# Kernel tuning notes

Measured on AMD Instinct MI355X. Metric: run time of the kernel, lower is better.

Reference implementation:

```python
import jax, jax.numpy as jnp
import numpy as np
from jax import lax

# Geometry constants (mirror ParallelGeometry with angle_ratio=1.0)
PHI_SIZE = 720
T_SIZE = 1024
N = 256            # reco_shape
B = 16             # batch
RHO = float(np.sqrt(2.0))          # ||max_pt - min_pt||/2 for [-1,1]^2
DT = 2.0 * RHO / T_SIZE            # detector step
A = -RHO                           # left edge used in phase factor
DPHI = np.pi / PHI_SIZE            # mean angle step (angle_ratio=1)


def setup_inputs() -> dict:
    key = jax.random.key(0)
    k1, k2, k3 = jax.random.split(key, 3)
    sinos = jax.random.normal(k1, (B, PHI_SIZE, T_SIZE), dtype=jnp.float32)
    kernel_re = jax.random.normal(k2, (T_SIZE // 2 + 1,), dtype=jnp.float32)
    kernel_im = jax.random.normal(k3, (T_SIZE // 2 + 1,), dtype=jnp.float32)
    return {"sinos": sinos, "kernel_re": kernel_re, "kernel_im": kernel_im}


def _filter_sinos(sinos, kernel):
    # fourier_transform (no padding): dt * exp(-i a w) * rfft(sinos)
    omgs = 2.0 * np.pi * jnp.fft.rfftfreq(T_SIZE, d=DT).astype(jnp.float32)  # [T/2+1]
    phase = jnp.exp(-1j * (A * omgs))          # cos(a w) - i sin(a w)
    sino_hat = (DT * phase) * jnp.fft.rfft(sinos, axis=-1)
    filtered_hat = kernel * sino_hat
    # inverse_fourier_transform: exp(+i a w)/dt * filtered_hat, then irfft
    back = (jnp.conj(phase) / DT) * filtered_hat
    return jnp.fft.irfft(back, n=T_SIZE, axis=-1)   # [B, phi, T], real


def _backproject(filtered):
    # Parallel-beam backprojection (ODL RayTransform adjoint):
    # f(x,y) = dphi * sum_phi lin_interp(g[phi], t = x cos(phi) + y sin(phi))
    angles = ((jnp.arange(PHI_SIZE, dtype=jnp.float32) + 0.5) * (np.pi / PHI_SIZE))
    xs = (-1.0 + (jnp.arange(N, dtype=jnp.float32) + 0.5) * (2.0 / N))  # pixel centers
    X, Y = jnp.meshgrid(xs, xs, indexing='ij')      # ODL axis order: [x, y]
    g_seq = jnp.transpose(filtered, (1, 0, 2))      # [phi, B, T]

    def step(acc, inp):
        g, phi = inp                                # g: [B, T]
        t = X * jnp.cos(phi) + Y * jnp.sin(phi)     # [N, N], always in [-rho, rho]
        u = (t + RHO) / DT - 0.5                    # fractional detector index
        i0 = jnp.clip(jnp.floor(u).astype(jnp.int32), 0, T_SIZE - 2)
        w = u - i0.astype(jnp.float32)
        val = g[:, i0] * (1.0 - w) + g[:, i0 + 1] * w   # [B, N, N]
        return acc + val, None

    acc0 = jnp.zeros((filtered.shape[0], N, N), dtype=filtered.dtype)
    acc, _ = lax.scan(step, acc0, (g_seq, angles))
    return acc * jnp.asarray(DPHI, dtype=filtered.dtype)


def reference(sinos, kernel_re, kernel_im):
    kernel = kernel_re.astype(jnp.complex64) + 1j * kernel_im.astype(jnp.complex64)
    filtered = _filter_sinos(sinos, kernel)
    return _backproject(filtered)
```

## Files before the change

### kernel.cpp

```cpp
#include <hip/hip_runtime.h>

#define PHI 720
#define TS 1024
#define NB 16
#define NPIX 256

#define INVDT 362.03867196751236f
#define DXF 0.0078125f
#define DPHI_F 0.0043633231299858237f

#define WS_TW 0
#define WS_ANG 4096
#define WS_PT 8192
#define WS_NEEDED (8192 + 256 * 360 * 16)

__device__ __forceinline__ float2 cmulf2(float2 a, float2 b) {
    return make_float2(a.x * b.x - a.y * b.y, a.x * b.y + a.y * b.x);
}
__device__ __forceinline__ float fract_fast(float x) {
#if __has_builtin(__builtin_amdgcn_fractf)
    return __builtin_amdgcn_fractf(x);
#else
    return x - floorf(x);
#endif
}

__global__ __launch_bounds__(256) void precompute_kernel(char* __restrict__ wsb) {
    const int blk = blockIdx.x, tid = threadIdx.x;
    if (blk < 360) {
        const int e = blk * 256 + tid;
        const unsigned repu = (unsigned)e / 360u;
        const int rep = (int)repu;
        const int a = e - rep * 360;
        const int ti = rep >> 4, tj = rep & 15;
        float s, c;
        sincosf(((float)a + 0.5f) * (3.14159265358979323846f / 720.0f), &s, &c);
        const float x0 = -1.0f + ((float)(ti * 8) + 0.5f) * DXF;
        const float x7 = x0 + 7.0f * DXF;
        const float y0 = -1.0f + ((float)(tj * 8) + 0.5f) * DXF;
        const float y7 = y0 + 7.0f * DXF;
        const float uTmin = (c * x0 + s * y0) * INVDT + 511.5f;
        const float uTmax = (c * x7 + s * y7) * INVDT + 511.5f;
        const float uUmin = (s * x0 - c * y7) * INVDT + 511.5f;
        const float uUmax = (s * x7 - c * y0) * INVDT + 511.5f;
        int wbA = (int)floorf(uTmin - 0.02f) - 1;
        int wbB = (int)floorf(1023.0f - uTmax - 0.02f) - 1;
        int wbC = (int)floorf(uUmin - 0.02f) - 1;
        int wbD = (int)floorf(1023.0f - uUmax - 0.02f) - 1;
        wbA = min(max(wbA, 0), 992);
        wbB = min(max(wbB, 0), 992);
        wbC = min(max(wbC, 0), 992);
        wbD = min(max(wbD, 0), 992);
        uint4 ent;
        ent.x = __float_as_uint(511.5f - (float)wbA);
        ent.y = __float_as_uint(511.5f - (float)wbC);
        ent.z = (unsigned)wbA | ((unsigned)wbB << 16);
        ent.w = (unsigned)wbC | ((unsigned)wbD << 16);
        ((uint4*)(wsb + WS_PT))[e] = ent;
    } else if (blk < 362) {
        const int k = (blk - 360) * 256 + tid;
        float s, c;
        sincosf((float)k * (6.28318530717958647692f / 1024.0f), &s, &c);
        ((float2*)(wsb + WS_TW))[k] = make_float2(c, -s);
    } else {
        const int a = (blk - 362) * 256 + tid;
        if (a < 360) {
            float s, c;
            sincosf(((float)a + 0.5f) * (3.14159265358979323846f / 720.0f), &s, &c);
            ((float2*)(wsb + WS_ANG))[a] = make_float2(c * INVDT, s * INVDT);
        }
    }
}

__device__ __forceinline__ void r4_stage(const float2* __restrict__ s0, float2* __restrict__ d0,
                                         const float2* __restrict__ s1, float2* __restrict__ d1,
                                         const float2* __restrict__ tw, int tid, int m, bool inv) {
    const int q = tid & ~(m - 1);
    const int o = tid + 3 * q;
    float2 w1 = tw[q], w2 = tw[2 * q];
    if (inv) { w1.y = -w1.y; w2.y = -w2.y; }
    #pragma unroll
    for (int f = 0; f < 2; ++f) {
        const float2* s = f ? s1 : s0;
        float2* d = f ? d1 : d0;
        const float2 a = s[tid], b = s[tid + 256], c = s[tid + 512], e = s[tid + 768];
        const float2 A = make_float2(a.x + c.x, a.y + c.y);
        const float2 Bm = cmulf2(w1, make_float2(a.x - c.x, a.y - c.y));
        const float2 C = make_float2(b.x + e.x, b.y + e.y);
        const float2 Dm = cmulf2(w1, make_float2(b.x - e.x, b.y - e.y));
        const float2 D = inv ? make_float2(-Dm.y, Dm.x) : make_float2(Dm.y, -Dm.x);
        d[o]         = make_float2(A.x + C.x, A.y + C.y);
        d[o + m]     = make_float2(Bm.x + D.x, Bm.y + D.y);
        d[o + 2 * m] = cmulf2(w2, make_float2(A.x - C.x, A.y - C.y));
        d[o + 3 * m] = cmulf2(w2, make_float2(Bm.x - D.x, Bm.y - D.y));
    }
}

__global__ __launch_bounds__(256) void filter_fft_kernel(float* __restrict__ sinos,
                                                         const float* __restrict__ kr,
                                                         const float* __restrict__ ki,
                                                         const char* __restrict__ wsb) {
    __shared__ float2 bufA[2][1024];
    __shared__ float2 bufB[2][1024];
    __shared__ float2 tw[512];
    const int tid = threadIdx.x;
    const int wg = blockIdx.x;
    const int lb = (wg & 7) * 360 + (wg >> 3);
    float* base = sinos + (size_t)lb * 4096;

    #pragma unroll
    for (int f = 0; f < 2; ++f) {
        float* r0 = base + f * 2048;
        float* r1 = r0 + 1024;
        #pragma unroll
        for (int h = 0; h < 4; ++h) {
            const int k = tid + h * 256;
            bufA[f][k] = make_float2(r0[k], r1[k]);
        }
    }
    if (wsb) {
        const float2* tg = (const float2*)(wsb + WS_TW);
        tw[tid] = tg[tid];
        tw[tid + 256] = tg[tid + 256];
    } else {
        #pragma unroll
        for (int h = 0; h < 2; ++h) {
            const int k = tid + h * 256;
            float s, c;
            sincosf((float)k * (6.28318530717958647692f / 1024.0f), &s, &c);
            tw[k] = make_float2(c, -s);
        }
    }
    __syncthreads();

    r4_stage(bufA[0], bufB[0], bufA[1], bufB[1], tw, tid, 1, false);   __syncthreads();
    r4_stage(bufB[0], bufA[0], bufB[1], bufA[1], tw, tid, 4, false);   __syncthreads();
    r4_stage(bufA[0], bufB[0], bufA[1], bufB[1], tw, tid, 16, false);  __syncthreads();
    r4_stage(bufB[0], bufA[0], bufB[1], bufA[1], tw, tid, 64, false);  __syncthreads();
    r4_stage(bufA[0], bufB[0], bufA[1], bufB[1], tw, tid, 256, false); __syncthreads();

    const float scale = DPHI_F / 1024.0f;
    #pragma unroll
    for (int h = 0; h < 4; ++h) {
        const int k = tid + h * 256;
        const int kk = (k <= 512) ? k : (1024 - k);
        const float re = kr[kk] * scale;
        float im = ((k == 0) || (k == 512)) ? 0.0f : ki[kk] * scale;
        if (k > 512) im = -im;
        #pragma unroll
        for (int f = 0; f < 2; ++f) {
            const float2 z = bufB[f][k];
            bufB[f][k] = make_float2(re * z.x - im * z.y, re * z.y + im * z.x);
        }
    }
    __syncthreads();

    r4_stage(bufB[0], bufA[0], bufB[1], bufA[1], tw, tid, 1, true);   __syncthreads();
    r4_stage(bufA[0], bufB[0], bufA[1], bufB[1], tw, tid, 4, true);   __syncthreads();
    r4_stage(bufB[0], bufA[0], bufB[1], bufA[1], tw, tid, 16, true);  __syncthreads();
    r4_stage(bufA[0], bufB[0], bufA[1], bufB[1], tw, tid, 64, true);  __syncthreads();
    r4_stage(bufB[0], bufA[0], bufB[1], bufA[1], tw, tid, 256, true); __syncthreads();

    #pragma unroll
    for (int f = 0; f < 2; ++f) {
        float* r0 = base + f * 2048;
        float* r1 = r0 + 1024;
        #pragma unroll
        for (int h = 0; h < 4; ++h) {
            const int k = tid + h * 256;
            const float2 v = bufA[f][k];
            r0[k] = v.x;
            r1[k] = v.y;
        }
    }
}

__global__ __launch_bounds__(64, 4) void backproj_sym_kernel(const float* __restrict__ filt,
                                                             float* __restrict__ out,
                                                             const char* __restrict__ wsb) {
    __shared__ float lds[2 * 4 * 256];
    const int l = threadIdx.x;
    const int wg = blockIdx.x;
    const int lb = ((wg & 7) << 9) | (wg >> 3);
    const int b = lb >> 8;
    const int rep = lb & 255;
    const int ti = rep >> 4, tj = rep & 15;

    const float2* __restrict__ ang = (const float2*)(wsb + WS_ANG);
    const uint4* __restrict__ pt = ((const uint4*)(wsb + WS_PT)) + rep * 360;

    const int ii = l >> 3, jj = l & 7;
    const int ip = ti * 8 + ii, jp = tj * 8 + jj;
    const float Xc = -1.0f + ((float)ip + 0.5f) * DXF;
    const float Yc = -1.0f + ((float)jp + 0.5f) * DXF;
    const int vbyte = ((l & 31) + ((l >> 5) * (360 * 1024))) * 4;
    const float* __restrict__ gb = filt + (size_t)b * (PHI * TS);

    float a0 = 0.f, a1 = 0.f, a2 = 0.f, a3 = 0.f;
    float pf[4][4];

#define STAGE(CH) { \
    _Pragma("unroll") \
    for (int p = 0; p < 4; ++p) { \
        const int ap = (CH) * 4 + p; \
        const uint4 e = pt[ap]; \
        const char* rp = (const char*)(gb + (ap << 10)); \
        pf[p][0] = *(const float*)(rp + ((e.z & 0xFFFFu) << 2) + vbyte); \
        pf[p][1] = *(const float*)(rp + ((e.z >> 16) << 2) + vbyte); \
        pf[p][2] = *(const float*)(rp + ((e.w & 0xFFFFu) << 2) + vbyte); \
        pf[p][3] = *(const float*)(rp + ((e.w >> 16) << 2) + vbyte); \
    } }

#define WRITE(BUF) { \
    _Pragma("unroll") \
    for (int p = 0; p < 4; ++p) { \
        _Pragma("unroll") \
        for (int w = 0; w < 4; ++w) \
            lds[(BUF) * 1024 + p * 256 + w * 64 + l] = pf[p][w]; \
    } }

#define COMPUTE(BUF, CH) { \
    _Pragma("unroll") \
    for (int p = 0; p < 4; ++p) { \
        const int ap = (CH) * 4 + p; \
        const uint4 e = pt[ap]; \
        const float2 cs = ang[ap]; \
        const float* slot = &lds[(BUF) * 1024 + p * 256]; \
        const float kFA = __uint_as_float(e.x), kFC = __uint_as_float(e.y); \
        const int wbA = (int)(e.z & 0xFFFFu), wbB = (int)(e.z >> 16); \
        const int wbC = (int)(e.w & 0xFFFFu), wbD = (int)(e.w >> 16); \
        const float uT = fmaf(cs.x, Xc, fmaf(cs.y, Yc, kFA)); \
        const float uU = fmaf(cs.y, Xc, fmaf(cs.x, -Yc, kFC)); \
        const int iA = (int)uT; const float wT = fract_fast(uT); \
        const int iC = (int)uU; const float wU = fract_fast(uU); \
        const int iB = 1022 - wbA - wbB - iA; \
        const int iD = 1022 - wbC - wbD - iC; \
        { const float g0 = slot[iA],       g1 = slot[iA + 1]; \
          const float h0 = slot[iA + 32],  h1 = slot[iA + 33]; \
          a0 = fmaf(wT, g1 - g0, a0 + g0); a1 = fmaf(wT, h1 - h0, a1 + h0); } \
        { const float g0 = slot[64 + iB],  g1 = slot[65 + iB]; \
          const float h0 = slot[96 + iB],  h1 = slot[97 + iB]; \
          a2 = fmaf(wT, g0 - g1, a2 + g1); a3 = fmaf(wT, h0 - h1, a3 + h1); } \
        { const float g0 = slot[128 + iC], g1 = slot[129 + iC]; \
          const float h0 = slot[160 + iC], h1 = slot[161 + iC]; \
          a1 = fmaf(wU, g1 - g0, a1 + g0); a2 = fmaf(wU, h1 - h0, a2 + h0); } \
        { const float g0 = slot[192 + iD], g1 = slot[193 + iD]; \
          const float h0 = slot[224 + iD], h1 = slot[225 + iD]; \
          a3 = fmaf(wU, g0 - g1, a3 + g1); a0 = fmaf(wU, h0 - h1, a0 + h1); } \
    } }

    STAGE(0); WRITE(0);
    for (int cc = 0; cc < 44; ++cc) {
        STAGE(2 * cc + 1);
        COMPUTE(0, 2 * cc);
        WRITE(1);
        STAGE(2 * cc + 2);
        COMPUTE(1, 2 * cc + 1);
        WRITE(0);
    }
    STAGE(89);
    COMPUTE(0, 88);
    WRITE(1);
    COMPUTE(1, 89);

#undef STAGE
#undef WRITE
#undef COMPUTE

    const int bb = b << 8;
    out[((size_t)((bb + ip) << 8)) + jp]                    = a0;
    out[((size_t)((bb + 255 - jp) << 8)) + ip]              = a1;
    out[((size_t)((bb + 255 - ip) << 8)) + (255 - jp)]      = a2;
    out[((size_t)((bb + jp) << 8)) + (255 - ip)]            = a3;
}

__global__ __launch_bounds__(256) void backproj_fb_kernel(const float* __restrict__ filt,
                                                          float* __restrict__ out) {
    __shared__ float2 csI[PHI];
    __shared__ float win[8 * 128];
    __shared__ float woffF[8];

    const int tid = threadIdx.x;
    const int wg = blockIdx.x;
    const int lb = ((wg & 7) << 7) | (wg >> 3);
    const int b = lb >> 6;
    const int tile = lb & 63;
    const int i0 = (tile >> 3) * 32;
    const int j0 = (tile & 7) * 32;

    for (int p = tid; p < PHI; p += 256) {
        const float angv = ((float)p + 0.5f) * (float)(3.14159265358979323846 / 720.0);
        float s, c;
        sincosf(angv, &s, &c);
        csI[p] = make_float2(c * INVDT, s * INVDT);
    }

    const int lane = tid & 63;
    const int wv = tid >> 6;
    const int ii = lane & 7;
    const int jj = lane >> 3;
    const int ipx = i0 + ii;
    const int j = j0 + wv * 8 + jj;

    const float Xc = -1.0f + ((float)ipx + 0.5f) * DXF;
    const float Yc = -1.0f + ((float)j + 0.5f) * DXF;

    const int r = tid >> 5;
    const int l32 = tid & 31;
    const float xlo = -1.0f + ((float)i0 + 0.5f) * DXF;
    const float xhi = -1.0f + ((float)i0 + 31.5f) * DXF;
    const float ylo = -1.0f + ((float)j0 + 0.5f) * DXF;
    const float yhi = -1.0f + ((float)j0 + 31.5f) * DXF;

    const float* gb = filt + (size_t)b * PHI * TS;
    float acc0 = 0.f, acc1 = 0.f, acc2 = 0.f, acc3 = 0.f;

    __syncthreads();

    {
        const float2 cs = csI[r];
        const float um = fminf(cs.x * xlo, cs.x * xhi) + fminf(cs.y * ylo, cs.y * yhi) + 511.5f;
        const int wb = (int)floorf(um) - 1;
        const float* grow = gb + (size_t)r * TS;
        #pragma unroll
        for (int h = 0; h < 4; ++h) {
            int gi = wb + l32 + 32 * h;
            gi = gi < 0 ? 0 : (gi > TS - 1 ? TS - 1 : gi);
            win[r * 128 + l32 + 32 * h] = grow[gi];
        }
        if (l32 == 0) woffF[r] = 511.5f + (float)(r * 128 - wb);
    }
    __syncthreads();

    for (int c = 0; c < PHI / 8; ++c) {
        float gp0 = 0.f, gp1 = 0.f, gp2 = 0.f, gp3 = 0.f;
        int wbn = 0;
        const bool more = (c + 1 < PHI / 8);
        if (more) {
            const int a = (c + 1) * 8 + r;
            const float2 cs = csI[a];
            const float um = fminf(cs.x * xlo, cs.x * xhi) + fminf(cs.y * ylo, cs.y * yhi) + 511.5f;
            wbn = (int)floorf(um) - 1;
            const float* grow = gb + (size_t)a * TS;
            int g0 = wbn + l32;      g0 = g0 < 0 ? 0 : (g0 > TS - 1 ? TS - 1 : g0);
            int g1 = wbn + l32 + 32; g1 = g1 < 0 ? 0 : (g1 > TS - 1 ? TS - 1 : g1);
            int g2 = wbn + l32 + 64; g2 = g2 < 0 ? 0 : (g2 > TS - 1 ? TS - 1 : g2);
            int g3 = wbn + l32 + 96; g3 = g3 < 0 ? 0 : (g3 > TS - 1 ? TS - 1 : g3);
            gp0 = grow[g0]; gp1 = grow[g1]; gp2 = grow[g2]; gp3 = grow[g3];
        }
        #pragma unroll
        for (int aa = 0; aa < 8; ++aa) {
            const float2 cs = csI[c * 8 + aa];
            const float offF = woffF[aa];
            float u = fmaf(cs.y, Yc, cs.x * Xc) + offF;
            const float dup = cs.x * 0.0625f;
            #pragma unroll
            for (int p = 0; p < 4; ++p) {
                const int idx = (int)u;
                const float wf = fract_fast(u);
                const float g0 = win[idx], g1 = win[idx + 1];
                if (p == 0) acc0 = fmaf(wf, g1 - g0, acc0 + g0);
                else if (p == 1) acc1 = fmaf(wf, g1 - g0, acc1 + g0);
                else if (p == 2) acc2 = fmaf(wf, g1 - g0, acc2 + g0);
                else acc3 = fmaf(wf, g1 - g0, acc3 + g0);
                u += dup;
            }
        }
        __syncthreads();
        if (more) {
            win[r * 128 + l32] = gp0;
            win[r * 128 + l32 + 32] = gp1;
            win[r * 128 + l32 + 64] = gp2;
            win[r * 128 + l32 + 96] = gp3;
            if (l32 == 0) woffF[r] = 511.5f + (float)(r * 128 - wbn);
        }
        __syncthreads();
    }

    const size_t ob = ((size_t)(b * NPIX + ipx)) * NPIX + j;
    out[ob] = acc0;
    out[ob + 8 * NPIX] = acc1;
    out[ob + 16 * NPIX] = acc2;
    out[ob + 24 * NPIX] = acc3;
}

extern "C" void kernel_launch(void* const* d_in, const int* in_sizes, int n_in,
                              void* d_out, int out_size, void* d_ws, size_t ws_size,
                              hipStream_t stream) {
    float* sinos = (float*)d_in[0];
    const float* kr = (const float*)d_in[1];
    const float* ki = (const float*)d_in[2];
    float* out = (float*)d_out;

    char* wsb = nullptr;
    if (ws_size >= (size_t)WS_NEEDED && d_ws != nullptr) {
        wsb = (char*)d_ws;
        precompute_kernel<<<364, 256, 0, stream>>>(wsb);
    }
    filter_fft_kernel<<<NB * PHI / 4, 256, 0, stream>>>(sinos, kr, ki, wsb);
    if (wsb) {
        backproj_sym_kernel<<<4096, 64, 0, stream>>>(sinos, out, wsb);
    } else {
        backproj_fb_kernel<<<NB * 64, 256, 0, stream>>>(sinos, out);
    }
}
```

Before: 291.0 us.

## Split backprojection angles across two waves with atomics; fuse filter into first inverse FFT stage

Result: faster. 265.1 us (-8.9%).

```diff
diff --git a/kernel.cpp b/kernel.cpp
--- a/kernel.cpp
+++ b/kernel.cpp
@@ -96,6 +96,15 @@
     }
 }
 
+__device__ __forceinline__ float2 kfac(const float* __restrict__ kr,
+                                       const float* __restrict__ ki, int k, float scale) {
+    const int kk = (k <= 512) ? k : (1024 - k);
+    const float re = kr[kk] * scale;
+    float im = ((k == 0) || (k == 512)) ? 0.0f : ki[kk] * scale;
+    if (k > 512) im = -im;
+    return make_float2(re, im);
+}
+
 __global__ __launch_bounds__(256) void filter_fft_kernel(float* __restrict__ sinos,
                                                          const float* __restrict__ kr,
                                                          const float* __restrict__ ki,
@@ -139,23 +148,37 @@
     r4_stage(bufB[0], bufA[0], bufB[1], bufA[1], tw, tid, 64, false);  __syncthreads();
     r4_stage(bufA[0], bufB[0], bufA[1], bufB[1], tw, tid, 256, false); __syncthreads();
 
-    const float scale = DPHI_F / 1024.0f;
-    #pragma unroll
-    for (int h = 0; h < 4; ++h) {
-        const int k = tid + h * 256;
-        const int kk = (k <= 512) ? k : (1024 - k);
-        const float re = kr[kk] * scale;
-        float im = ((k == 0) || (k == 512)) ? 0.0f : ki[kk] * scale;
-        if (k > 512) im = -im;
+    {
+        const float scale = DPHI_F / 1024.0f;
+        const int q = tid;
+        const int o = 4 * tid;
+        float2 w1 = tw[q], w2 = tw[2 * q];
+        w1.y = -w1.y; w2.y = -w2.y;
+        const float2 f0 = kfac(kr, ki, tid, scale);
+        const float2 f1 = kfac(kr, ki, tid + 256, scale);
+        const float2 f2 = kfac(kr, ki, tid + 512, scale);
+        const float2 f3 = kfac(kr, ki, tid + 768, scale);
         #pragma unroll
         for (int f = 0; f < 2; ++f) {
-            const float2 z = bufB[f][k];
-            bufB[f][k] = make_float2(re * z.x - im * z.y, re * z.y + im * z.x);
+            const float2* s = bufB[f];
+            float2* d = bufA[f];
+            const float2 a = cmulf2(f0, s[tid]);
+            const float2 b = cmulf2(f1, s[tid + 256]);
+            const float2 c = cmulf2(f2, s[tid + 512]);
+            const float2 e = cmulf2(f3, s[tid + 768]);
+            const float2 A = make_float2(a.x + c.x, a.y + c.y);
+            const float2 Bm = cmulf2(w1, make_float2(a.x - c.x, a.y - c.y));
+            const float2 C = make_float2(b.x + e.x, b.y + e.y);
+            const float2 Dm = cmulf2(w1, make_float2(b.x - e.x, b.y - e.y));
+            const float2 D = make_float2(-Dm.y, Dm.x);
+            d[o]     = make_float2(A.x + C.x, A.y + C.y);
+            d[o + 1] = make_float2(Bm.x + D.x, Bm.y + D.y);
+            d[o + 2] = cmulf2(w2, make_float2(A.x - C.x, A.y - C.y));
+            d[o + 3] = cmulf2(w2, make_float2(Bm.x - D.x, Bm.y - D.y));
         }
     }
     __syncthreads();
 
-    r4_stage(bufB[0], bufA[0], bufB[1], bufA[1], tw, tid, 1, true);   __syncthreads();
     r4_stage(bufA[0], bufB[0], bufA[1], bufB[1], tw, tid, 4, true);   __syncthreads();
     r4_stage(bufB[0], bufA[0], bufB[1], bufA[1], tw, tid, 16, true);  __syncthreads();
     r4_stage(bufA[0], bufB[0], bufA[1], bufB[1], tw, tid, 64, true);  __syncthreads();
@@ -175,11 +198,13 @@
     }
 }
 
-__global__ __launch_bounds__(64, 4) void backproj_sym_kernel(const float* __restrict__ filt,
-                                                             float* __restrict__ out,
-                                                             const char* __restrict__ wsb) {
-    __shared__ float lds[2 * 4 * 256];
-    const int l = threadIdx.x;
+__global__ __launch_bounds__(128, 8) void backproj_sym_kernel(const float* __restrict__ filt,
+                                                              float* __restrict__ out,
+                                                              const char* __restrict__ wsb) {
+    __shared__ float lds[2048];
+    const int tid = threadIdx.x;
+    const int hf = __builtin_amdgcn_readfirstlane(tid >> 6);
+    const int l = tid & 63;
     const int wg = blockIdx.x;
     const int lb = ((wg & 7) << 9) | (wg >> 3);
     const int b = lb >> 8;
@@ -195,14 +220,15 @@
     const float Yc = -1.0f + ((float)jp + 0.5f) * DXF;
     const int vbyte = ((l & 31) + ((l >> 5) * (360 * 1024))) * 4;
     const float* __restrict__ gb = filt + (size_t)b * (PHI * TS);
+    const int lbase = hf * 1024;
 
     float a0 = 0.f, a1 = 0.f, a2 = 0.f, a3 = 0.f;
-    float pf[4][4];
+    float pf[2][4];
 
 #define STAGE(CH) { \
     _Pragma("unroll") \
-    for (int p = 0; p < 4; ++p) { \
-        const int ap = (CH) * 4 + p; \
+    for (int p = 0; p < 2; ++p) { \
+        const int ap = hf * 180 + (CH) * 2 + p; \
         const uint4 e = pt[ap]; \
         const char* rp = (const char*)(gb + (ap << 10)); \
         pf[p][0] = *(const float*)(rp + ((e.z & 0xFFFFu) << 2) + vbyte); \
@@ -213,40 +239,44 @@
 
 #define WRITE(BUF) { \
     _Pragma("unroll") \
-    for (int p = 0; p < 4; ++p) { \
+    for (int p = 0; p < 2; ++p) { \
         _Pragma("unroll") \
         for (int w = 0; w < 4; ++w) \
-            lds[(BUF) * 1024 + p * 256 + w * 64 + l] = pf[p][w]; \
+            lds[lbase + (BUF) * 512 + p * 256 + w * 64 + l] = pf[p][w]; \
     } }
 
 #define COMPUTE(BUF, CH) { \
     _Pragma("unroll") \
-    for (int p = 0; p < 4; ++p) { \
-        const int ap = (CH) * 4 + p; \
+    for (int p = 0; p < 2; ++p) { \
+        const int ap = hf * 180 + (CH) * 2 + p; \
         const uint4 e = pt[ap]; \
         const float2 cs = ang[ap]; \
-        const float* slot = &lds[(BUF) * 1024 + p * 256]; \
+        const float* slot = &lds[lbase + (BUF) * 512 + p * 256]; \
         const float kFA = __uint_as_float(e.x), kFC = __uint_as_float(e.y); \
         const int wbA = (int)(e.z & 0xFFFFu), wbB = (int)(e.z >> 16); \
         const int wbC = (int)(e.w & 0xFFFFu), wbD = (int)(e.w >> 16); \
         const float uT = fmaf(cs.x, Xc, fmaf(cs.y, Yc, kFA)); \
         const float uU = fmaf(cs.y, Xc, fmaf(cs.x, -Yc, kFC)); \
-        const int iA = (int)uT; const float wT = fract_fast(uT); \
-        const int iC = (int)uU; const float wU = fract_fast(uU); \
+        const int iA = (int)uT; const float wT = fract_fast(uT); const float oT = 1.0f - wT; \
+        const int iC = (int)uU; const float wU = fract_fast(uU); const float oU = 1.0f - wU; \
         const int iB = 1022 - wbA - wbB - iA; \
         const int iD = 1022 - wbC - wbD - iC; \
         { const float g0 = slot[iA],       g1 = slot[iA + 1]; \
           const float h0 = slot[iA + 32],  h1 = slot[iA + 33]; \
-          a0 = fmaf(wT, g1 - g0, a0 + g0); a1 = fmaf(wT, h1 - h0, a1 + h0); } \
+          a0 = fmaf(g0, oT, a0); a0 = fmaf(g1, wT, a0); \
+          a1 = fmaf(h0, oT, a1); a1 = fmaf(h1, wT, a1); } \
         { const float g0 = slot[64 + iB],  g1 = slot[65 + iB]; \
           const float h0 = slot[96 + iB],  h1 = slot[97 + iB]; \
-          a2 = fmaf(wT, g0 - g1, a2 + g1); a3 = fmaf(wT, h0 - h1, a3 + h1); } \
+          a2 = fmaf(g1, oT, a2); a2 = fmaf(g0, wT, a2); \
+          a3 = fmaf(h1, oT, a3); a3 = fmaf(h0, wT, a3); } \
         { const float g0 = slot[128 + iC], g1 = slot[129 + iC]; \
           const float h0 = slot[160 + iC], h1 = slot[161 + iC]; \
-          a1 = fmaf(wU, g1 - g0, a1 + g0); a2 = fmaf(wU, h1 - h0, a2 + h0); } \
+          a1 = fmaf(g0, oU, a1); a1 = fmaf(g1, wU, a1); \
+          a2 = fmaf(h0, oU, a2); a2 = fmaf(h1, wU, a2); } \
         { const float g0 = slot[192 + iD], g1 = slot[193 + iD]; \
           const float h0 = slot[224 + iD], h1 = slot[225 + iD]; \
-          a3 = fmaf(wU, g0 - g1, a3 + g1); a0 = fmaf(wU, h0 - h1, a0 + h1); } \
+          a3 = fmaf(g1, oU, a3); a3 = fmaf(g0, wU, a3); \
+          a0 = fmaf(h1, oU, a0); a0 = fmaf(h0, wU, a0); } \
     } }
 
     STAGE(0); WRITE(0);
@@ -268,10 +298,10 @@
 #undef COMPUTE
 
     const int bb = b << 8;
-    out[((size_t)((bb + ip) << 8)) + jp]                    = a0;
-    out[((size_t)((bb + 255 - jp) << 8)) + ip]              = a1;
-    out[((size_t)((bb + 255 - ip) << 8)) + (255 - jp)]      = a2;
-    out[((size_t)((bb + jp) << 8)) + (255 - ip)]            = a3;
+    atomicAdd(&out[((size_t)((bb + ip) << 8)) + jp], a0);
+    atomicAdd(&out[((size_t)((bb + 255 - jp) << 8)) + ip], a1);
+    atomicAdd(&out[((size_t)((bb + 255 - ip) << 8)) + (255 - jp)], a2);
+    atomicAdd(&out[((size_t)((bb + jp) << 8)) + (255 - ip)], a3);
 }
 
 __global__ __launch_bounds__(256) void backproj_fb_kernel(const float* __restrict__ filt,
@@ -399,7 +429,8 @@
     }
     filter_fft_kernel<<<NB * PHI / 4, 256, 0, stream>>>(sinos, kr, ki, wsb);
     if (wsb) {
-        backproj_sym_kernel<<<4096, 64, 0, stream>>>(sinos, out, wsb);
+        hipMemsetAsync(d_out, 0, (size_t)out_size * sizeof(float), stream);
+        backproj_sym_kernel<<<4096, 128, 0, stream>>>(sinos, out, wsb);
     } else {
         backproj_fb_kernel<<<NB * 64, 256, 0, stream>>>(sinos, out);
     }
```
